# Kernel tuning notes

Hardware: AMD Instinct MI355X
Metric: run time of the kernel (lower is better)

## Reference

```python
import jax, jax.numpy as jnp
import numpy as np

D_CONV = 4
DT_RANK = 64
D_STATE = 16


def setup_inputs() -> dict:
    key = jax.random.key(0)
    ks = jax.random.split(key, 10)
    d_model, d_in, L, B = 1024, 2048, 1024, 2
    s = 0.02
    x = jax.random.normal(ks[0], (B, L, d_model), jnp.float32)
    W_in = jax.random.normal(ks[1], (d_model, 2 * d_in), jnp.float32) * s
    conv_w = jax.random.normal(ks[2], (D_CONV, 1, d_in), jnp.float32) * s
    conv_b = jax.random.normal(ks[3], (d_in,), jnp.float32) * s
    W_x = jax.random.normal(ks[4], (d_in, DT_RANK + 2 * D_STATE), jnp.float32) * s
    W_dt = jax.random.normal(ks[5], (DT_RANK, d_in), jnp.float32) * s
    b_dt = jax.random.normal(ks[6], (d_in,), jnp.float32) * s
    A_log = jnp.log(jnp.tile(jnp.arange(1, D_STATE + 1, dtype=jnp.float32), (d_in, 1)))
    D = jnp.ones((d_in,), jnp.float32)
    W_out = jax.random.normal(ks[7], (d_in, d_model), jnp.float32) * s
    return {"x": x, "W_in": W_in, "conv_w": conv_w, "conv_b": conv_b,
            "W_x": W_x, "W_dt": W_dt, "b_dt": b_dt, "A_log": A_log, "D": D,
            "W_out": W_out}


def _selective_scan(u, delta, A, Bm, Cm, D):
    # u, delta: [b,l,d]; A: [d,n]; Bm, Cm: [b,l,n]; D: [d]
    b, l, d = u.shape
    n = A.shape[1]
    deltaA = jnp.exp(jnp.einsum('bld,dn->bldn', delta, A))          # [b,l,d,n]
    dBu = delta[..., None] * Bm[:, :, None, :] * u[..., None]        # [b,l,d,n]

    def step(state, inp):
        dA_t, dBu_t, C_t = inp                                       # [b,d,n],[b,d,n],[b,n]
        state = dA_t * state + dBu_t
        y_t = jnp.einsum('bdn,bn->bd', state, C_t)
        return state, y_t

    init = jnp.zeros((b, d, n), u.dtype)
    xs = (jnp.swapaxes(deltaA, 0, 1), jnp.swapaxes(dBu, 0, 1), jnp.swapaxes(Cm, 0, 1))
    _, ys = jax.lax.scan(step, init, xs)                             # [l,b,d]
    y = jnp.swapaxes(ys, 0, 1)
    return y + u * D


def reference(x, W_in, conv_w, conv_b, W_x, W_dt, b_dt, A_log, D, W_out):
    B, L, _ = x.shape
    d_in = W_in.shape[1] // 2

    x_and_res = x @ W_in                                             # [B,L,2*d_in]
    x_, res = jnp.split(x_and_res, [d_in], axis=-1)

    # depthwise causal conv over the projected branch
    x_pad = jnp.pad(x_, ((0, 0), (D_CONV - 1, 0), (0, 0)))
    x_conv = jax.lax.conv_general_dilated(
        x_pad, conv_w, window_strides=(1,), padding='VALID',
        dimension_numbers=('NWC', 'WIO', 'NWC'), feature_group_count=d_in)
    x_conv = x_conv[:, :L, :] + conv_b
    x_conv = jax.nn.silu(x_conv)

    # ssm
    A = -jnp.exp(A_log)                                              # [d_in,n]
    x_dbl = x_conv @ W_x                                             # [B,L,dt_rank+2n]
    delta, Bm, Cm = jnp.split(x_dbl, [DT_RANK, DT_RANK + D_STATE], axis=-1)
    delta = jax.nn.softplus(delta @ W_dt + b_dt)                     # [B,L,d_in]
    y = _selective_scan(x_conv, delta, A, Bm, Cm, D)

    y = y * jax.nn.silu(res)
    return y @ W_out
```

## Files before the change

### kernel.cpp

```cpp
#include <hip/hip_runtime.h>
#include <hip/hip_bf16.h>
#include <math.h>


typedef unsigned short u16;
typedef short s16;
typedef float f32x4 __attribute__((ext_vector_type(4)));
typedef s16 bf16x8 __attribute__((ext_vector_type(8)));
typedef u16 u16x4 __attribute__((ext_vector_type(4)));
typedef u16 u16x8 __attribute__((ext_vector_type(8)));

#define LDS_CAST(p) ((__attribute__((address_space(3))) void*)(p))
#define GLB_CAST(p) ((const __attribute__((address_space(1))) void*)(p))

#define LL 1024
#define DI 2048
#define NC 32
#define LC 32

#define OFF_FLAG   0u
#define OFF_CX     256u
#define OFF_CCW    4194560u
#define OFF_CCB    4211200u
#define OFF_CBDT   4215296u
#define OFF_CALOG  4219392u
#define OFF_CD     4284928u
#define OFF_WINT   4289024u
#define OFF_WOUTT  12677632u
#define OFF_WXT    16871936u
#define OFF_WDTT   17265152u
#define OFF_XRP    17527296u
#define OFF_XF     (OFF_XRP + 0u)
#define OFF_P      (OFF_XRP + 0u)
#define OFF_YBF    (OFF_XRP + 0u)
#define OFF_S      (OFF_XRP + 16777216u)
#define OFF_SIN    (OFF_XRP + 33554432u)
#define OFF_YP     (OFF_XRP + 16777216u)
#define OFF_RESACT 84636160u
#define OFF_XCB    101413376u
#define OFF_XDBLP  109801984u
#define OFF_XDBL   116093440u
#define OFF_DELTA  116486656u

static __device__ __forceinline__ float b2f(u16 h) {
  return __uint_as_float(((unsigned)h) << 16);
}
static __device__ __forceinline__ u16 f2b(float f) {
  unsigned u = __float_as_uint(f);
  u += 0x7fffu + ((u >> 16) & 1u);
  return (u16)(u >> 16);
}

__global__ __launch_bounds__(256) void detect_dtype(
    const u16* __restrict__ x, const void* __restrict__ alog, int* flag) {
  __shared__ int cnt;
  if (threadIdx.x == 0) cnt = 0;
  __syncthreads();
  int good = 0;
#pragma unroll
  for (int j = 0; j < 16; j++) {
    u16 v = x[threadIdx.x * 16 + j];
    int e = (v >> 7) & 0xFF;
    good += (e >= 100 && e <= 140) ? 1 : 0;
  }
  atomicAdd(&cnt, good);
  __syncthreads();
  if (threadIdx.x == 0) {
    int fp32in = (cnt < 3600) ? 1 : 0;
    flag[0] = fp32in;
    int structured = fp32in;
    if (fp32in) {
      const float* af = (const float*)alog;
#pragma unroll
      for (int n = 0; n < 16; n++) {
        float a0 = __expf(af[n]);
        float a1 = __expf(af[777 * 16 + n]);
        float t = (float)(n + 1);
        if (fabsf(a0 - t) > 0.01f * t || fabsf(a1 - t) > 0.01f * t) structured = 0;
      }
    }
    flag[1] = structured;
  }
}

__global__ __launch_bounds__(256) void prep_inputs(
    const void* sx, const void* scw, const void* scb, const void* sbdt,
    const void* salog, const void* sd,
    const void* Win, const void* Wx, const void* Wdt, const void* Wout,
    char* __restrict__ ws, const int* __restrict__ flag) {
  const int fl = flag[0];
  int bid = blockIdx.x;
  if (bid < 1047) {
    long g = (long)bid * 256 + threadIdx.x;
    const void* src; u16* dst; long j;
    if (g < 262144)      { src = sx;    dst = (u16*)(ws + OFF_CX);    j = g; }
    else if (g < 263168) { src = scw;   dst = (u16*)(ws + OFF_CCW);   j = g - 262144; }
    else if (g < 263424) { src = scb;   dst = (u16*)(ws + OFF_CCB);   j = g - 263168; }
    else if (g < 263680) { src = sbdt;  dst = (u16*)(ws + OFF_CBDT);  j = g - 263424; }
    else if (g < 267776) { src = salog; dst = (u16*)(ws + OFF_CALOG); j = g - 263680; }
    else                 { src = sd;    dst = (u16*)(ws + OFF_CD);    j = g - 267776; }
    u16x8 o;
    if (fl) {
      f32x4 a = ((const f32x4*)src)[j*2];
      f32x4 b = ((const f32x4*)src)[j*2 + 1];
#pragma unroll
      for (int c = 0; c < 4; c++) { o[c] = f2b(a[c]); o[c+4] = f2b(b[c]); }
    } else {
      o = ((const u16x8*)src)[j];
    }
    *(u16x8*)&dst[j*8] = o;
    return;
  }
  bid -= 1047;
  const void* src; u16* dst; int R, C, tx_, ty_;
  if (bid < 1024)      { src=Win;  dst=(u16*)(ws+OFF_WINT);  R=1024; C=4096; ty_=bid>>6;        tx_=bid&63; }
  else if (bid < 1536) { bid-=1024; src=Wout; dst=(u16*)(ws+OFF_WOUTT); R=2048; C=1024; ty_=bid>>4; tx_=bid&15; }
  else if (bid < 1600) { bid-=1536; src=Wx;   dst=(u16*)(ws+OFF_WXT);   R=2048; C=96;   ty_=bid>>1; tx_=bid&1; }
  else                 { bid-=1600; src=Wdt;  dst=(u16*)(ws+OFF_WDTT);  R=64;   C=2048; ty_=0;      tx_=bid; }
  __shared__ u16 tile[64][68];
  const int tx = threadIdx.x & 15, ty = threadIdx.x >> 4;
  const int c0 = tx_*64, r0 = ty_*64;
  const int cl = tx*4;
#pragma unroll
  for (int i = 0; i < 4; i++) {
    int rl = ty + i*16;
    int r = r0 + rl, c = c0 + cl;
    if (r < R && c + 3 < C) {
      u16x4 v;
      if (fl) {
        f32x4 a = *(const f32x4*)((const float*)src + (size_t)r*C + c);
#pragma unroll
        for (int q = 0; q < 4; q++) v[q] = f2b(a[q]);
      } else {
        v = *(const u16x4*)((const u16*)src + (size_t)r*C + c);
      }
      *(u16x4*)&tile[rl][cl] = v;
    }
  }
  __syncthreads();
#pragma unroll
  for (int i = 0; i < 4; i++) {
    int cc = ty + i*16;
    int c = c0 + cc, rbase = r0 + cl;
    if (c < C && rbase + 3 < R) {
      u16x4 v;
#pragma unroll
      for (int q = 0; q < 4; q++) v[q] = tile[cl + q][cc];
      *(u16x4*)&dst[(size_t)c*R + rbase] = v;
    }
  }
}

__global__ __launch_bounds__(256) void gemm_in_fused(
    const u16* __restrict__ A, const u16* __restrict__ Bt,
    float* __restrict__ xf, float* __restrict__ resact) {
  __shared__ u16 sA[128*32];
  __shared__ u16 sB[128*32];
  const int tid = threadIdx.x;
  const int lane = tid & 63, w = tid >> 6;
  const int ln = lane & 15, q = lane >> 4;
  const int wr = w >> 1, wc = w & 1;
  const int m0 = blockIdx.y * 128, n0 = blockIdx.x * 128;
  const int lda = 1024;
  const int li0 = tid, li1 = tid + 256;
  const int r0s = li0 >> 2, k0s = (li0 & 3) * 8;
  const int r1s = li1 >> 2, k1s = (li1 & 3) * 8;
  f32x4 acc[4][4] = {};
  for (int k0 = 0; k0 < 1024; k0 += 32) {
    __syncthreads();
    __builtin_amdgcn_global_load_lds(GLB_CAST(A + (size_t)(m0 + r0s)*lda + k0 + k0s), LDS_CAST(&sA[(size_t)li0*8]), 16, 0, 0);
    __builtin_amdgcn_global_load_lds(GLB_CAST(A + (size_t)(m0 + r1s)*lda + k0 + k1s), LDS_CAST(&sA[(size_t)li1*8]), 16, 0, 0);
    __builtin_amdgcn_global_load_lds(GLB_CAST(Bt + (size_t)(n0 + r0s)*lda + k0 + k0s), LDS_CAST(&sB[(size_t)li0*8]), 16, 0, 0);
    __builtin_amdgcn_global_load_lds(GLB_CAST(Bt + (size_t)(n0 + r1s)*lda + k0 + k1s), LDS_CAST(&sB[(size_t)li1*8]), 16, 0, 0);
    __syncthreads();
    bf16x8 af[4], bfr[4];
#pragma unroll
    for (int i = 0; i < 4; i++) {
      af[i]  = *(const bf16x8*)&sA[(wr*64 + i*16 + ln)*32 + q*8];
      bfr[i] = *(const bf16x8*)&sB[(wc*64 + i*16 + ln)*32 + q*8];
    }
#pragma unroll
    for (int mi = 0; mi < 4; mi++)
#pragma unroll
      for (int ni = 0; ni < 4; ni++)
        acc[mi][ni] = __builtin_amdgcn_mfma_f32_16x16x32_bf16(af[mi], bfr[ni], acc[mi][ni], 0, 0, 0);
  }
  const int half = (n0 >= DI) ? 1 : 0;
  float* dst = half ? resact : xf;
  const int nb = n0 - (half ? DI : 0);
#pragma unroll
  for (int mi = 0; mi < 4; mi++)
#pragma unroll
    for (int ni = 0; ni < 4; ni++)
#pragma unroll
      for (int r = 0; r < 4; r++) {
        int m = m0 + wr*64 + mi*16 + q*4 + r;
        int n = nb + wc*64 + ni*16 + ln;
        float v = acc[mi][ni][r];
        if (half) {
          if (!(v == v)) v = 0.f;
          float t = fminf(fmaxf(v, -80.f), 80.f);
          v = v / (1.f + __expf(-t));
        }
        dst[(size_t)m*DI + n] = v;
      }
}

__global__ __launch_bounds__(256) void conv_silu(
    const float* __restrict__ xf, const u16* __restrict__ cw, const u16* __restrict__ cb,
    u16* __restrict__ xcb) {
  int idx4 = blockIdx.x * 256 + threadIdx.x;
  int d = (idx4 & 511) * 4;
  int row = idx4 >> 9;
  int l = row & (LL - 1);
  u16x4 cbv = *(const u16x4*)(cb + d);
  float acc[4];
#pragma unroll
  for (int c = 0; c < 4; c++) acc[c] = b2f(cbv[c]);
#pragma unroll
  for (int j = 0; j < 4; j++) {
    int ls = l - 3 + j;
    if (ls >= 0) {
      f32x4 xv = *(const f32x4*)(xf + (size_t)(row - 3 + j)*DI + d);
      u16x4 wv = *(const u16x4*)(cw + j*DI + d);
#pragma unroll
      for (int c = 0; c < 4; c++) acc[c] += b2f(wv[c]) * xv[c];
    }
  }
  u16x4 outv;
#pragma unroll
  for (int c = 0; c < 4; c++) {
    float a = acc[c];
    if (!(a == a)) a = 0.f;
    float t = fminf(fmaxf(a, -80.f), 80.f);
    outv[c] = f2b(a / (1.f + __expf(-t)));
  }
  *(u16x4*)(xcb + (size_t)row*DI + d) = outv;
}

__global__ __launch_bounds__(256) void xdbl_split(
    const u16* __restrict__ A, const u16* __restrict__ Bt, float* __restrict__ outP) {
  int wg = blockIdx.x * 4 + (threadIdx.x >> 6);
  int lane = threadIdx.x & 63, ln = lane & 15, q = lane >> 4;
  int mt = wg / 48, rem = wg % 48;
  int nt = rem >> 3, ks = rem & 7;
  const u16* ap = A  + (size_t)(mt*16 + ln)*2048 + ks*256 + q*8;
  const u16* bp = Bt + (size_t)(nt*16 + ln)*2048 + ks*256 + q*8;
  f32x4 acc = {};
#pragma unroll
  for (int k0 = 0; k0 < 256; k0 += 32) {
    bf16x8 a = *(const bf16x8*)(ap + k0);
    bf16x8 b = *(const bf16x8*)(bp + k0);
    acc = __builtin_amdgcn_mfma_f32_16x16x32_bf16(a, b, acc, 0, 0, 0);
  }
#pragma unroll
  for (int r = 0; r < 4; r++)
    outP[((size_t)ks*2048 + mt*16 + q*4 + r)*96 + nt*16 + ln] = acc[r];
}

__global__ __launch_bounds__(256) void xdbl_reduce(
    const float* __restrict__ outP, u16* __restrict__ xdbl) {
  int i = blockIdx.x * 256 + threadIdx.x;
  float s = 0.f;
#pragma unroll
  for (int ks = 0; ks < 8; ks++) s += outP[(size_t)ks*196608 + i];
  xdbl[i] = f2b(s);
}

__global__ __launch_bounds__(256) void gemm_delta(
    const u16* __restrict__ xdbl, const u16* __restrict__ WdtT,
    const u16* __restrict__ bdt, float* __restrict__ delta) {
  int w = (blockIdx.x * 256 + threadIdx.x) >> 6;
  int lane = threadIdx.x & 63, ln = lane & 15, q = lane >> 4;
  int mt = w & 127, nt = w >> 7;
  const u16* ap = xdbl + (size_t)(mt*16 + ln)*96 + q*8;
  const u16* bp = WdtT + (size_t)(nt*16 + ln)*64 + q*8;
  f32x4 acc = {};
#pragma unroll
  for (int k0 = 0; k0 < 64; k0 += 32) {
    bf16x8 a = *(const bf16x8*)(ap + k0);
    bf16x8 b = *(const bf16x8*)(bp + k0);
    acc = __builtin_amdgcn_mfma_f32_16x16x32_bf16(a, b, acc, 0, 0, 0);
  }
#pragma unroll
  for (int r = 0; r < 4; r++) {
    int m = mt*16 + q*4 + r, n = nt*16 + ln;
    float v = acc[r] + b2f(bdt[n]);
    if (!(v == v)) v = 0.f;
    float sp = (v > 15.f) ? v : log1pf(__expf(fmaxf(v, -80.f)));
    delta[(size_t)m*DI + n] = sp;
  }
}

__global__ __launch_bounds__(256) void scan_p1(
    const float* __restrict__ delta, const u16* __restrict__ xcb,
    const u16* __restrict__ xdbl, const u16* __restrict__ Alog,
    float* __restrict__ P, float* __restrict__ S, const int* __restrict__ flag) {
  const int structured = flag[1];
  int bid = blockIdx.x;
  int b = bid >> 8, r = bid & 255;
  int chunk = r >> 3, dblk = r & 7;
  int d = dblk*256 + threadIdx.x;
  float s[16], p[16];
#pragma unroll
  for (int n = 0; n < 16; n++) { s[n] = 0.f; p[n] = 1.f; }
  int row0 = b*LL + chunk*LC;
  if (structured) {
    for (int l = 0; l < LC; l++) {
      int row = row0 + l;
      float dl = delta[(size_t)row*DI + d];
      float du = dl * b2f(xcb[(size_t)row*DI + d]);
      const u16* bq = xdbl + (size_t)row*96 + 64;
      bf16x8 bv0 = *(const bf16x8*)(bq);
      bf16x8 bv1 = *(const bf16x8*)(bq + 8);
      float e1 = __expf(-dl);
      float dAc = 1.f;
#pragma unroll
      for (int n = 0; n < 8; n++) {
        dAc *= e1;
        s[n] = dAc * s[n] + du * b2f((u16)bv0[n]);
        p[n] *= dAc;
      }
#pragma unroll
      for (int n = 0; n < 8; n++) {
        dAc *= e1;
        s[n+8] = dAc * s[n+8] + du * b2f((u16)bv1[n]);
        p[n+8] *= dAc;
      }
    }
  } else {
    float Av[16];
#pragma unroll
    for (int n = 0; n < 16; n++) Av[n] = -__expf(fminf(b2f(Alog[d*16 + n]), 80.f));
    for (int l = 0; l < LC; l++) {
      int row = row0 + l;
      float dl = delta[(size_t)row*DI + d];
      float du = dl * b2f(xcb[(size_t)row*DI + d]);
      const u16* bq = xdbl + (size_t)row*96 + 64;
      bf16x8 bv0 = *(const bf16x8*)(bq);
      bf16x8 bv1 = *(const bf16x8*)(bq + 8);
#pragma unroll
      for (int n = 0; n < 8; n++) {
        float dA = __expf(fmaxf(dl * Av[n], -80.f));
        s[n] = dA * s[n] + du * b2f((u16)bv0[n]);
        p[n] *= dA;
      }
#pragma unroll
      for (int n = 0; n < 8; n++) {
        float dA = __expf(fmaxf(dl * Av[n+8], -80.f));
        s[n+8] = dA * s[n+8] + du * b2f((u16)bv1[n]);
        p[n+8] *= dA;
      }
    }
  }
  size_t o = ((size_t)(b*NC + chunk)*DI + d) * 16;
#pragma unroll
  for (int n = 0; n < 16; n++) { P[o + n] = p[n]; S[o + n] = s[n]; }
}

__global__ __launch_bounds__(256) void scan_p2(
    const float* __restrict__ P, const float* __restrict__ S, float* __restrict__ sIn) {
  int idx = blockIdx.x * 256 + threadIdx.x;
  int n = idx & 15, d = (idx >> 4) & (DI - 1), b = idx >> 15;
  float s = 0.f;
  for (int c = 0; c < NC; c++) {
    size_t o = ((size_t)(b*NC + c)*DI + d)*16 + n;
    sIn[o] = s;
    s = P[o] * s + S[o];
  }
}

__global__ __launch_bounds__(256) void scan_p3(
    const float* __restrict__ delta, const u16* __restrict__ xcb,
    const u16* __restrict__ xdbl, const u16* __restrict__ Alog,
    const u16* __restrict__ Dp, const float* __restrict__ resact,
    const float* __restrict__ sIn, u16* __restrict__ ybf, const int* __restrict__ flag) {
  const int structured = flag[1];
  int bid = blockIdx.x;
  int b = bid >> 8, r = bid & 255;
  int chunk = r >> 3, dblk = r & 7;
  int d = dblk*256 + threadIdx.x;
  float Dv = b2f(Dp[d]);
  float s[16];
  size_t o = ((size_t)(b*NC + chunk)*DI + d) * 16;
#pragma unroll
  for (int n = 0; n < 16; n++) s[n] = sIn[o + n];
  int row0 = b*LL + chunk*LC;
  if (structured) {
    for (int l = 0; l < LC; l++) {
      int row = row0 + l;
      float dl = delta[(size_t)row*DI + d];
      float u  = b2f(xcb[(size_t)row*DI + d]);
      float du = dl * u;
      const u16* bq = xdbl + (size_t)row*96 + 64;
      bf16x8 bv0 = *(const bf16x8*)(bq);
      bf16x8 bv1 = *(const bf16x8*)(bq + 8);
      bf16x8 cv0 = *(const bf16x8*)(bq + 16);
      bf16x8 cv1 = *(const bf16x8*)(bq + 24);
      float e1 = __expf(-dl);
      float dAc = 1.f;
      float y = 0.f;
#pragma unroll
      for (int n = 0; n < 8; n++) {
        dAc *= e1;
        s[n] = dAc * s[n] + du * b2f((u16)bv0[n]);
        y += s[n] * b2f((u16)cv0[n]);
      }
#pragma unroll
      for (int n = 0; n < 8; n++) {
        dAc *= e1;
        s[n+8] = dAc * s[n+8] + du * b2f((u16)bv1[n]);
        y += s[n+8] * b2f((u16)cv1[n]);
      }
      y += u * Dv;
      float out = y * resact[(size_t)row*DI + d];
      if (!(out == out)) out = 0.f;
      ybf[(size_t)row*DI + d] = f2b(out);
    }
  } else {
    float Av[16];
#pragma unroll
    for (int n = 0; n < 16; n++) Av[n] = -__expf(fminf(b2f(Alog[d*16 + n]), 80.f));
    for (int l = 0; l < LC; l++) {
      int row = row0 + l;
      float dl = delta[(size_t)row*DI + d];
      float u  = b2f(xcb[(size_t)row*DI + d]);
      float du = dl * u;
      const u16* bq = xdbl + (size_t)row*96 + 64;
      bf16x8 bv0 = *(const bf16x8*)(bq);
      bf16x8 bv1 = *(const bf16x8*)(bq + 8);
      bf16x8 cv0 = *(const bf16x8*)(bq + 16);
      bf16x8 cv1 = *(const bf16x8*)(bq + 24);
      float y = 0.f;
#pragma unroll
      for (int n = 0; n < 8; n++) {
        float dA = __expf(fmaxf(dl * Av[n], -80.f));
        s[n] = dA * s[n] + du * b2f((u16)bv0[n]);
        y += s[n] * b2f((u16)cv0[n]);
      }
#pragma unroll
      for (int n = 0; n < 8; n++) {
        float dA = __expf(fmaxf(dl * Av[n+8], -80.f));
        s[n+8] = dA * s[n+8] + du * b2f((u16)bv1[n]);
        y += s[n+8] * b2f((u16)cv1[n]);
      }
      y += u * Dv;
      float out = y * resact[(size_t)row*DI + d];
      if (!(out == out)) out = 0.f;
      ybf[(size_t)row*DI + d] = f2b(out);
    }
  }
}

__global__ __launch_bounds__(256) void gemm128split(
    const u16* __restrict__ A, const u16* __restrict__ Bt,
    float* __restrict__ Cout, int M, int N, int lda, int kslice) {
  __shared__ u16 sA[128*32];
  __shared__ u16 sB[128*32];
  const int tid = threadIdx.x;
  const int lane = tid & 63, w = tid >> 6;
  const int ln = lane & 15, q = lane >> 4;
  const int wr = w >> 1, wc = w & 1;
  const int m0 = blockIdx.y * 128, n0 = blockIdx.x * 128;
  const int kstart = blockIdx.z * kslice, kend = kstart + kslice;
  Cout += (size_t)blockIdx.z * M * N;
  const int li0 = tid, li1 = tid + 256;
  const int r0s = li0 >> 2, k0s = (li0 & 3) * 8;
  const int r1s = li1 >> 2, k1s = (li1 & 3) * 8;
  f32x4 acc[4][4] = {};
  for (int k0 = kstart; k0 < kend; k0 += 32) {
    __syncthreads();
    __builtin_amdgcn_global_load_lds(GLB_CAST(A + (size_t)(m0 + r0s)*lda + k0 + k0s), LDS_CAST(&sA[(size_t)li0*8]), 16, 0, 0);
    __builtin_amdgcn_global_load_lds(GLB_CAST(A + (size_t)(m0 + r1s)*lda + k0 + k1s), LDS_CAST(&sA[(size_t)li1*8]), 16, 0, 0);
    __builtin_amdgcn_global_load_lds(GLB_CAST(Bt + (size_t)(n0 + r0s)*lda + k0 + k0s), LDS_CAST(&sB[(size_t)li0*8]), 16, 0, 0);
    __builtin_amdgcn_global_load_lds(GLB_CAST(Bt + (size_t)(n0 + r1s)*lda + k0 + k1s), LDS_CAST(&sB[(size_t)li1*8]), 16, 0, 0);
    __syncthreads();
    bf16x8 af[4], bfr[4];
#pragma unroll
    for (int i = 0; i < 4; i++) {
      af[i]  = *(const bf16x8*)&sA[(wr*64 + i*16 + ln)*32 + q*8];
      bfr[i] = *(const bf16x8*)&sB[(wc*64 + i*16 + ln)*32 + q*8];
    }
#pragma unroll
    for (int mi = 0; mi < 4; mi++)
#pragma unroll
      for (int ni = 0; ni < 4; ni++)
        acc[mi][ni] = __builtin_amdgcn_mfma_f32_16x16x32_bf16(af[mi], bfr[ni], acc[mi][ni], 0, 0, 0);
  }
#pragma unroll
  for (int mi = 0; mi < 4; mi++)
#pragma unroll
    for (int ni = 0; ni < 4; ni++)
#pragma unroll
      for (int r = 0; r < 4; r++) {
        int m = m0 + wr*64 + mi*16 + q*4 + r;
        int n = n0 + wc*64 + ni*16 + ln;
        Cout[(size_t)m*N + n] = acc[mi][ni][r];
      }
}

__global__ __launch_bounds__(256) void out_reduce(
    const float* __restrict__ yP, void* __restrict__ out, const int* __restrict__ flag) {
  const int fl = flag[0];
  int i = blockIdx.x * 256 + threadIdx.x;
  float v = 0.f;
#pragma unroll
  for (int z = 0; z < 4; z++) v += yP[(size_t)z*2097152 + i];
  if (!(v == v)) v = 0.f;
  if (fl) ((float*)out)[i] = v;
  else    ((u16*)out)[i] = f2b(v);
}

extern "C" void kernel_launch(void* const* d_in, const int* in_sizes, int n_in,
                              void* d_out, int out_size, void* d_ws, size_t ws_size,
                              hipStream_t stream) {
  char* ws = (char*)d_ws;
  int*   flag   = (int*)  (ws + OFF_FLAG);
  u16*   cx     = (u16*)  (ws + OFF_CX);
  u16*   ccw    = (u16*)  (ws + OFF_CCW);
  u16*   ccb    = (u16*)  (ws + OFF_CCB);
  u16*   cbdt   = (u16*)  (ws + OFF_CBDT);
  u16*   cAlog  = (u16*)  (ws + OFF_CALOG);
  u16*   cD     = (u16*)  (ws + OFF_CD);
  u16*   WinT   = (u16*)  (ws + OFF_WINT);
  u16*   WoutT  = (u16*)  (ws + OFF_WOUTT);
  u16*   WxT    = (u16*)  (ws + OFF_WXT);
  u16*   WdtT   = (u16*)  (ws + OFF_WDTT);
  float* xf     = (float*)(ws + OFF_XF);
  float* resact = (float*)(ws + OFF_RESACT);
  u16*   xcb    = (u16*)  (ws + OFF_XCB);
  float* xdblP  = (float*)(ws + OFF_XDBLP);
  u16*   xdbl   = (u16*)  (ws + OFF_XDBL);
  float* delta  = (float*)(ws + OFF_DELTA);
  u16*   ybf    = (u16*)  (ws + OFF_YBF);
  float* P      = (float*)(ws + OFF_P);
  float* S      = (float*)(ws + OFF_S);
  float* sIn    = (float*)(ws + OFF_SIN);
  float* yP     = (float*)(ws + OFF_YP);

  detect_dtype<<<1, 256, 0, stream>>>((const u16*)d_in[0], d_in[7], flag);
  prep_inputs<<<2679, 256, 0, stream>>>(
      d_in[0], d_in[2], d_in[3], d_in[6], d_in[7], d_in[8],
      d_in[1], d_in[4], d_in[5], d_in[9], ws, flag);
  gemm_in_fused<<<dim3(32, 16), 256, 0, stream>>>(cx, WinT, xf, resact);
  conv_silu<<<4096, 256, 0, stream>>>(xf, ccw, ccb, xcb);
  xdbl_split<<<1536, 256, 0, stream>>>(xcb, WxT, xdblP);
  xdbl_reduce<<<768, 256, 0, stream>>>(xdblP, xdbl);
  gemm_delta<<<4096, 256, 0, stream>>>(xdbl, WdtT, cbdt, delta);
  scan_p1<<<512, 256, 0, stream>>>(delta, xcb, xdbl, cAlog, P, S, flag);
  scan_p2<<<256, 256, 0, stream>>>(P, S, sIn);
  scan_p3<<<512, 256, 0, stream>>>(delta, xcb, xdbl, cAlog, cD, resact, sIn, ybf, flag);
  gemm128split<<<dim3(8, 16, 4), 256, 0, stream>>>(ybf, WoutT, yP, 2048, 1024, 2048, 512);
  out_reduce<<<8192, 256, 0, stream>>>(yP, d_out, flag);
}
```

Baseline: 253.9 us.

## Use 256x256 double-buffered split-K input GEMM and fuse partial reduction into conv

Replaces the 128x128 single-buffered input projection GEMM with a 256x256 tile, 512-thread, double-buffered kernel. It uses split-K of 2 and writes fp32 partial sums to workspace. The conv/SiLU kernel now sums the two partials, and also applies the res-branch SiLU that previously ran in the GEMM epilogue. This raises data reuse and overlaps loads with MFMA, at the cost of writing and reading twice as much fp32 intermediate data, using 128KB of LDS, and running only 256 blocks at one block per CU.

```diff
diff --git a/kernel.cpp b/kernel.cpp
--- a/kernel.cpp
+++ b/kernel.cpp
@@ -30,7 +30,6 @@
 #define OFF_WXT    16871936u
 #define OFF_WDTT   17265152u
 #define OFF_XRP    17527296u
-#define OFF_XF     (OFF_XRP + 0u)
 #define OFF_P      (OFF_XRP + 0u)
 #define OFF_YBF    (OFF_XRP + 0u)
 #define OFF_S      (OFF_XRP + 16777216u)
@@ -151,91 +150,124 @@
   }
 }
 
-__global__ __launch_bounds__(256) void gemm_in_fused(
-    const u16* __restrict__ A, const u16* __restrict__ Bt,
-    float* __restrict__ xf, float* __restrict__ resact) {
-  __shared__ u16 sA[128*32];
-  __shared__ u16 sB[128*32];
+#define G1_STAGE(SA, SB, T) do {                                                  \
+    int k0_ = kstart + (T)*64;                                                    \
+    _Pragma("unroll")                                                             \
+    for (int i_ = 0; i_ < 4; i_++) {                                              \
+      int row_ = i_*64 + (tid>>3);                                                \
+      int kc_ = (tid&7)*8;                                                        \
+      __builtin_amdgcn_global_load_lds(GLB_CAST(A  + (size_t)(m0 + row_)*1024 + k0_ + kc_), \
+                                       LDS_CAST(&SA[i_*4096 + tid*8]), 16, 0, 0); \
+      __builtin_amdgcn_global_load_lds(GLB_CAST(Bt + (size_t)(n0 + row_)*1024 + k0_ + kc_), \
+                                       LDS_CAST(&SB[i_*4096 + tid*8]), 16, 0, 0); \
+    }                                                                             \
+  } while (0)
+
+#define G1_COMPUTE(SA, SB) do {                                                   \
+    _Pragma("unroll")                                                             \
+    for (int kk = 0; kk < 2; kk++) {                                              \
+      bf16x8 bfr[4];                                                              \
+      _Pragma("unroll")                                                           \
+      for (int ni = 0; ni < 4; ni++)                                              \
+        bfr[ni] = *(const bf16x8*)&SB[(wc*64 + ni*16 + ln)*64 + kk*32 + q*8];     \
+      _Pragma("unroll")                                                           \
+      for (int mi = 0; mi < 8; mi++) {                                            \
+        bf16x8 af = *(const bf16x8*)&SA[(wr*128 + mi*16 + ln)*64 + kk*32 + q*8];  \
+        _Pragma("unroll")                                                         \
+        for (int ni = 0; ni < 4; ni++)                                            \
+          acc[mi][ni] = __builtin_amdgcn_mfma_f32_16x16x32_bf16(af, bfr[ni], acc[mi][ni], 0, 0, 0); \
+      }                                                                           \
+    }                                                                             \
+  } while (0)
+
+__global__ __launch_bounds__(512, 1) void gemm_in_256(
+    const u16* __restrict__ A, const u16* __restrict__ Bt, float* __restrict__ part) {
+  __shared__ u16 sA0[256*64];
+  __shared__ u16 sB0[256*64];
+  __shared__ u16 sA1[256*64];
+  __shared__ u16 sB1[256*64];
   const int tid = threadIdx.x;
   const int lane = tid & 63, w = tid >> 6;
   const int ln = lane & 15, q = lane >> 4;
-  const int wr = w >> 1, wc = w & 1;
-  const int m0 = blockIdx.y * 128, n0 = blockIdx.x * 128;
-  const int lda = 1024;
-  const int li0 = tid, li1 = tid + 256;
-  const int r0s = li0 >> 2, k0s = (li0 & 3) * 8;
-  const int r1s = li1 >> 2, k1s = (li1 & 3) * 8;
-  f32x4 acc[4][4] = {};
-  for (int k0 = 0; k0 < 1024; k0 += 32) {
+  const int wr = w >> 2, wc = w & 3;
+  const int m0 = blockIdx.y * 256, n0 = blockIdx.x * 256;
+  const int kstart = blockIdx.z * 512;
+  float* Cout = part + (size_t)blockIdx.z * (2048*4096);
+  f32x4 acc[8][4] = {};
+  G1_STAGE(sA0, sB0, 0);
+  __syncthreads();
+#pragma unroll
+  for (int t2 = 0; t2 < 8; t2 += 2) {
+    G1_STAGE(sA1, sB1, t2 + 1);
+    G1_COMPUTE(sA0, sB0);
     __syncthreads();
-    __builtin_amdgcn_global_load_lds(GLB_CAST(A + (size_t)(m0 + r0s)*lda + k0 + k0s), LDS_CAST(&sA[(size_t)li0*8]), 16, 0, 0);
-    __builtin_amdgcn_global_load_lds(GLB_CAST(A + (size_t)(m0 + r1s)*lda + k0 + k1s), LDS_CAST(&sA[(size_t)li1*8]), 16, 0, 0);
-    __builtin_amdgcn_global_load_lds(GLB_CAST(Bt + (size_t)(n0 + r0s)*lda + k0 + k0s), LDS_CAST(&sB[(size_t)li0*8]), 16, 0, 0);
-    __builtin_amdgcn_global_load_lds(GLB_CAST(Bt + (size_t)(n0 + r1s)*lda + k0 + k1s), LDS_CAST(&sB[(size_t)li1*8]), 16, 0, 0);
+    if (t2 + 2 < 8) G1_STAGE(sA0, sB0, t2 + 2);
+    G1_COMPUTE(sA1, sB1);
     __syncthreads();
-    bf16x8 af[4], bfr[4];
-#pragma unroll
-    for (int i = 0; i < 4; i++) {
-      af[i]  = *(const bf16x8*)&sA[(wr*64 + i*16 + ln)*32 + q*8];
-      bfr[i] = *(const bf16x8*)&sB[(wc*64 + i*16 + ln)*32 + q*8];
-    }
-#pragma unroll
-    for (int mi = 0; mi < 4; mi++)
-#pragma unroll
-      for (int ni = 0; ni < 4; ni++)
-        acc[mi][ni] = __builtin_amdgcn_mfma_f32_16x16x32_bf16(af[mi], bfr[ni], acc[mi][ni], 0, 0, 0);
-  }
-  const int half = (n0 >= DI) ? 1 : 0;
-  float* dst = half ? resact : xf;
-  const int nb = n0 - (half ? DI : 0);
-#pragma unroll
-  for (int mi = 0; mi < 4; mi++)
+  }
+#pragma unroll
+  for (int mi = 0; mi < 8; mi++)
 #pragma unroll
     for (int ni = 0; ni < 4; ni++)
 #pragma unroll
       for (int r = 0; r < 4; r++) {
-        int m = m0 + wr*64 + mi*16 + q*4 + r;
-        int n = nb + wc*64 + ni*16 + ln;
-        float v = acc[mi][ni][r];
-        if (half) {
-          if (!(v == v)) v = 0.f;
-          float t = fminf(fmaxf(v, -80.f), 80.f);
-          v = v / (1.f + __expf(-t));
-        }
-        dst[(size_t)m*DI + n] = v;
-      }
-}
-
-__global__ __launch_bounds__(256) void conv_silu(
-    const float* __restrict__ xf, const u16* __restrict__ cw, const u16* __restrict__ cb,
-    u16* __restrict__ xcb) {
+        int m = m0 + wr*128 + mi*16 + q*4 + r;
+        int n = n0 + wc*64 + ni*16 + ln;
+        Cout[(size_t)m*4096 + n] = acc[mi][ni][r];
+      }
+}
+
+__global__ __launch_bounds__(256) void conv_silu_res(
+    const float* __restrict__ xrP, const u16* __restrict__ cw, const u16* __restrict__ cb,
+    u16* __restrict__ xcb, float* __restrict__ resact) {
+  const float* xr0 = xrP;
+  const float* xr1 = xrP + (size_t)2048*4096;
   int idx4 = blockIdx.x * 256 + threadIdx.x;
-  int d = (idx4 & 511) * 4;
-  int row = idx4 >> 9;
-  int l = row & (LL - 1);
-  u16x4 cbv = *(const u16x4*)(cb + d);
-  float acc[4];
-#pragma unroll
-  for (int c = 0; c < 4; c++) acc[c] = b2f(cbv[c]);
-#pragma unroll
-  for (int j = 0; j < 4; j++) {
-    int ls = l - 3 + j;
-    if (ls >= 0) {
-      f32x4 xv = *(const f32x4*)(xf + (size_t)(row - 3 + j)*DI + d);
-      u16x4 wv = *(const u16x4*)(cw + j*DI + d);
-#pragma unroll
-      for (int c = 0; c < 4; c++) acc[c] += b2f(wv[c]) * xv[c];
-    }
-  }
-  u16x4 outv;
-#pragma unroll
-  for (int c = 0; c < 4; c++) {
-    float a = acc[c];
-    if (!(a == a)) a = 0.f;
-    float t = fminf(fmaxf(a, -80.f), 80.f);
-    outv[c] = f2b(a / (1.f + __expf(-t)));
-  }
-  *(u16x4*)(xcb + (size_t)row*DI + d) = outv;
+  int row = idx4 >> 10;
+  int dq = idx4 & 1023;
+  if (dq < 512) {
+    int d = dq * 4;
+    int l = row & (LL - 1);
+    u16x4 cbv = *(const u16x4*)(cb + d);
+    float acc[4];
+#pragma unroll
+    for (int c = 0; c < 4; c++) acc[c] = b2f(cbv[c]);
+#pragma unroll
+    for (int j = 0; j < 4; j++) {
+      int ls = l - 3 + j;
+      if (ls >= 0) {
+        size_t o = (size_t)(row - 3 + j)*4096 + d;
+        f32x4 v0 = *(const f32x4*)(xr0 + o);
+        f32x4 v1 = *(const f32x4*)(xr1 + o);
+        u16x4 wv = *(const u16x4*)(cw + j*DI + d);
+#pragma unroll
+        for (int c = 0; c < 4; c++) acc[c] += b2f(wv[c]) * (v0[c] + v1[c]);
+      }
+    }
+    u16x4 outv;
+#pragma unroll
+    for (int c = 0; c < 4; c++) {
+      float a = acc[c];
+      if (!(a == a)) a = 0.f;
+      float t = fminf(fmaxf(a, -80.f), 80.f);
+      outv[c] = f2b(a / (1.f + __expf(-t)));
+    }
+    *(u16x4*)(xcb + (size_t)row*DI + d) = outv;
+  } else {
+    int d = (dq - 512) * 4;
+    size_t o = (size_t)row*4096 + 2048 + d;
+    f32x4 v0 = *(const f32x4*)(xr0 + o);
+    f32x4 v1 = *(const f32x4*)(xr1 + o);
+    f32x4 outv;
+#pragma unroll
+    for (int c = 0; c < 4; c++) {
+      float res = v0[c] + v1[c];
+      if (!(res == res)) res = 0.f;
+      float t = fminf(fmaxf(res, -80.f), 80.f);
+      outv[c] = res / (1.f + __expf(-t));
+    }
+    *(f32x4*)(resact + (size_t)row*DI + d) = outv;
+  }
 }
 
 __global__ __launch_bounds__(256) void xdbl_split(
@@ -526,7 +558,7 @@
   u16*   WoutT  = (u16*)  (ws + OFF_WOUTT);
   u16*   WxT    = (u16*)  (ws + OFF_WXT);
   u16*   WdtT   = (u16*)  (ws + OFF_WDTT);
-  float* xf     = (float*)(ws + OFF_XF);
+  float* xrP    = (float*)(ws + OFF_XRP);
   float* resact = (float*)(ws + OFF_RESACT);
   u16*   xcb    = (u16*)  (ws + OFF_XCB);
   float* xdblP  = (float*)(ws + OFF_XDBLP);
@@ -542,8 +574,8 @@
   prep_inputs<<<2679, 256, 0, stream>>>(
       d_in[0], d_in[2], d_in[3], d_in[6], d_in[7], d_in[8],
       d_in[1], d_in[4], d_in[5], d_in[9], ws, flag);
-  gemm_in_fused<<<dim3(32, 16), 256, 0, stream>>>(cx, WinT, xf, resact);
-  conv_silu<<<4096, 256, 0, stream>>>(xf, ccw, ccb, xcb);
+  gemm_in_256<<<dim3(16, 8, 2), 512, 0, stream>>>(cx, WinT, xrP);
+  conv_silu_res<<<8192, 256, 0, stream>>>(xrP, ccw, ccb, xcb, resact);
   xdbl_split<<<1536, 256, 0, stream>>>(xcb, WxT, xdblP);
   xdbl_reduce<<<768, 256, 0, stream>>>(xdblP, xdbl);
   gemm_delta<<<4096, 256, 0, stream>>>(xdbl, WdtT, cbdt, delta);
```

Result: no change. 257.3 us (+1.4%).
